# Kernel optimization log

Hardware: AMD Instinct MI355X
Metric: run time of the kernel (lower is better)

## Reference

```python
import jax, jax.numpy as jnp
import numpy as np


def _others_idx(n):
    # idx[i] = all agent indices except i, in order (prev agents then next agents),
    # matching the torch cat([prev_agents_msgs, next_agents_msgs]) ordering.
    return np.array([[j for j in range(n) if j != i] for i in range(n)], dtype=np.int32)


def setup_inputs() -> dict:
    key = jax.random.key(0)
    ks = jax.random.split(key, 6)
    bs, T, n, msg_len, obs_dim, hidden = 64, 256, 8, 16, 128, 64
    in_dim = obs_dim + (n - 1) * msg_len  # 240
    return {
        "obs": jax.random.normal(ks[0], (bs, T, n, obs_dim), jnp.float32),
        "messages": jax.random.normal(ks[1], (bs, T, n, msg_len), jnp.float32),
        "W1": jax.random.normal(ks[2], (n, in_dim, hidden), jnp.float32) * 0.05,
        "b1": jax.random.normal(ks[3], (n, hidden), jnp.float32) * 0.05,
        "W2": jax.random.normal(ks[4], (n, hidden, 1), jnp.float32) * 0.05,
        "b2": jax.random.normal(ks[5], (n, 1), jnp.float32) * 0.05,
    }


def reference(obs, messages, W1, b1, W2, b2):
    bs, T, n, msg_len = messages.shape
    idx = jnp.asarray(_others_idx(n))  # [n, n-1]
    # For each agent i at time t>0: concat of all OTHER agents' messages at t-1.
    m_prev = messages[:, :-1]                      # [bs, T-1, n, msg_len]
    gathered = m_prev[:, :, idx]                   # [bs, T-1, n, n-1, msg_len]
    msgs = gathered.reshape(bs, T - 1, n, (n - 1) * msg_len)
    pad = jnp.zeros((bs, 1, n, (n - 1) * msg_len), msgs.dtype)  # t=0 has no prior msgs
    msgs = jnp.concatenate([pad, msgs], axis=1)    # [bs, T, n, (n-1)*msg_len]
    inputs = jnp.concatenate([obs, msgs], axis=3)  # [bs, T, n, in_dim]
    # Per-agent independent MLP critic: Linear -> ReLU -> Linear
    h = jax.nn.relu(jnp.einsum('btai,aih->btah', inputs, W1) + b1)
    q = jnp.einsum('btah,aho->btao', h, W2) + b2   # [bs, T, n, 1]
    return q
```

## Files before the change

kernel.cpp:

```cpp
#include <hip/hip_runtime.h>


#define NAGENTS 8
#define MSG_LEN 16
#define OBS_DIM 128
#define HIDDEN  64
#define IN_DIM  240
#define TT      256
#define ROWS    16384
#define KSTEPS  15
#define MTILE   256
#define NFRAG   (KSTEPS * 2 * 64 * 8)

typedef __attribute__((ext_vector_type(8)))  short bf16x8;
typedef __attribute__((ext_vector_type(16))) float f32x16;

__device__ __forceinline__ unsigned short f2bf(float x) {
    unsigned u = __float_as_uint(x);
    u += 0x7fffu + ((u >> 16) & 1u);
    return (unsigned short)(u >> 16);
}
__device__ __forceinline__ float bf2f(unsigned short h) {
    return __uint_as_float(((unsigned)h) << 16);
}

__global__ __launch_bounds__(512, 4) void accritic_mfma_kernel(
    const float* __restrict__ obs,
    const float* __restrict__ msgs,
    const float* __restrict__ W1,
    const float* __restrict__ b1,
    const float* __restrict__ W2,
    const float* __restrict__ b2,
    float* __restrict__ out)
{
    __shared__ unsigned short WH[NFRAG];
    __shared__ unsigned short WL[NFRAG];

    const int a   = blockIdx.y;
    const int tid = threadIdx.x;
    const float* __restrict__ w1a = W1 + (size_t)a * IN_DIM * HIDDEN;

#pragma unroll
    for (int i = 0; i < NFRAG / 512; ++i) {
        int e    = tid + i * 512;
        int j    = e & 7;
        int lane = (e >> 3) & 63;
        int nt   = (e >> 9) & 1;
        int ks   = e >> 10;
        int k    = ks * 16 + (lane >> 5) * 8 + j;
        int col  = nt * 32 + (lane & 31);
        float w  = w1a[k * HIDDEN + col];
        unsigned short h = f2bf(w);
        WH[e] = h;
        WL[e] = f2bf(w - bf2f(h));
    }
    __syncthreads();

    const int wv   = tid >> 6;
    const int lane = tid & 63;
    const int rl   = lane & 31;
    const int kg   = lane >> 5;
    const int r    = blockIdx.x * MTILE + wv * 32 + rl;
    const int t    = r & (TT - 1);
    const bool zmsg = (t == 0);
    const int  rs   = zmsg ? r : r - 1;

    const float* __restrict__ obsp = obs + ((size_t)r * NAGENTS + a) * OBS_DIM + kg * 8;
    const float* __restrict__ msgp = msgs + (size_t)rs * NAGENTS * MSG_LEN + kg * 8;

    f32x16 acc0, acc1;
#pragma unroll
    for (int i = 0; i < 16; ++i) { acc0[i] = 0.f; acc1[i] = 0.f; }

    const bf16x8* __restrict__ WH8 = reinterpret_cast<const bf16x8*>(WH);
    const bf16x8* __restrict__ WL8 = reinterpret_cast<const bf16x8*>(WL);

#pragma unroll
    for (int ks = 0; ks < KSTEPS; ++ks) {
        float4 f0, f1;
        if (ks < 8) {
            const float4* p = reinterpret_cast<const float4*>(obsp + ks * 16);
            f0 = p[0]; f1 = p[1];
        } else {
            int pidx = ks - 8;
            int jsrc = (pidx < a) ? pidx : pidx + 1;
            const float4* p = reinterpret_cast<const float4*>(msgp + jsrc * MSG_LEN);
            f0 = p[0]; f1 = p[1];
            if (zmsg) { f0 = make_float4(0.f, 0.f, 0.f, 0.f); f1 = f0; }
        }

        float xf[8] = { f0.x, f0.y, f0.z, f0.w, f1.x, f1.y, f1.z, f1.w };
        bf16x8 ahi, alo;
#pragma unroll
        for (int q = 0; q < 8; ++q) {
            unsigned short h = f2bf(xf[q]);
            ahi[q] = (short)h;
            alo[q] = (short)f2bf(xf[q] - bf2f(h));
        }

        bf16x8 bh0 = WH8[(ks * 2 + 0) * 64 + lane];
        bf16x8 bh1 = WH8[(ks * 2 + 1) * 64 + lane];
        bf16x8 bl0 = WL8[(ks * 2 + 0) * 64 + lane];
        bf16x8 bl1 = WL8[(ks * 2 + 1) * 64 + lane];

        acc0 = __builtin_amdgcn_mfma_f32_32x32x16_bf16(ahi, bh0, acc0, 0, 0, 0);
        acc1 = __builtin_amdgcn_mfma_f32_32x32x16_bf16(ahi, bh1, acc1, 0, 0, 0);
        acc0 = __builtin_amdgcn_mfma_f32_32x32x16_bf16(alo, bh0, acc0, 0, 0, 0);
        acc1 = __builtin_amdgcn_mfma_f32_32x32x16_bf16(alo, bh1, acc1, 0, 0, 0);
        acc0 = __builtin_amdgcn_mfma_f32_32x32x16_bf16(ahi, bl0, acc0, 0, 0, 0);
        acc1 = __builtin_amdgcn_mfma_f32_32x32x16_bf16(ahi, bl1, acc1, 0, 0, 0);
    }

    const int cl = lane & 31;
    const float b1v0 = b1[a * HIDDEN + cl];
    const float b1v1 = b1[a * HIDDEN + 32 + cl];
    const float w2v0 = W2[a * HIDDEN + cl];
    const float w2v1 = W2[a * HIDDEN + 32 + cl];
    const float b2v  = b2[a];

    float v[16];
#pragma unroll
    for (int i = 0; i < 16; ++i) {
        float h0 = fmaxf(acc0[i] + b1v0, 0.f);
        float h1 = fmaxf(acc1[i] + b1v1, 0.f);
        v[i] = h0 * w2v0 + h1 * w2v1;
    }
#pragma unroll
    for (int off = 16; off >= 1; off >>= 1) {
#pragma unroll
        for (int i = 0; i < 16; ++i) v[i] += __shfl_xor(v[i], off, 64);
    }

    if (cl == 0) {
        const int r0 = blockIdx.x * MTILE + wv * 32;
#pragma unroll
        for (int i = 0; i < 16; ++i) {
            int row = (i & 3) + 8 * (i >> 2) + 4 * kg;
            out[(size_t)(r0 + row) * NAGENTS + a] = v[i] + b2v;
        }
    }
}

extern "C" void kernel_launch(void* const* d_in, const int* in_sizes, int n_in,
                              void* d_out, int out_size, void* d_ws, size_t ws_size,
                              hipStream_t stream) {
    const float* obs  = (const float*)d_in[0];
    const float* msgs = (const float*)d_in[1];
    const float* W1   = (const float*)d_in[2];
    const float* b1   = (const float*)d_in[3];
    const float* W2   = (const float*)d_in[4];
    const float* b2   = (const float*)d_in[5];
    float* out = (float*)d_out;

    dim3 grid(ROWS / MTILE, NAGENTS);
    accritic_mfma_kernel<<<grid, dim3(512), 0, stream>>>(obs, msgs, W1, b1, W2, b2, out);
}
```

Baseline: 125.0 us.

## Restructure critic kernel with register-resident weights and prefetched LDS-staged input tiles

Each block now processes four 64-row tiles in sequence. It keeps the W1 hi/lo bf16 fragments in registers rather than LDS, and stages coalesced input loads through LDS as pre-split hi/lo bf16. The next tile's global loads are issued before the current tile's MFMAs so memory latency overlaps compute. The two N halves are split across waves and combined through a small shared buffer, and the hi part now uses truncation instead of rounding. The cost is much higher register pressure (weights plus prefetch buffers) and extra barriers per tile.

```diff
diff --git a/kernel.cpp b/kernel.cpp
--- a/kernel.cpp
+++ b/kernel.cpp
@@ -9,22 +9,114 @@
 #define TT      256
 #define ROWS    16384
 #define KSTEPS  15
-#define MTILE   256
-#define NFRAG   (KSTEPS * 2 * 64 * 8)
+#define MTILE   64
+#define ASTR    248
+#define TPB     4
+#define GX      (ROWS / (MTILE * TPB))
 
 typedef __attribute__((ext_vector_type(8)))  short bf16x8;
 typedef __attribute__((ext_vector_type(16))) float f32x16;
 
-__device__ __forceinline__ unsigned short f2bf(float x) {
+__device__ __forceinline__ unsigned short f2bf_rne(float x) {
     unsigned u = __float_as_uint(x);
     u += 0x7fffu + ((u >> 16) & 1u);
     return (unsigned short)(u >> 16);
 }
-__device__ __forceinline__ float bf2f(unsigned short h) {
-    return __uint_as_float(((unsigned)h) << 16);
+
+__device__ __forceinline__ void load_tile(float4 (&xv)[15],
+    const float* __restrict__ obs, const float* __restrict__ msgs,
+    int m0, int a, int tid)
+{
+#pragma unroll
+    for (int it = 0; it < 15; ++it) {
+        int f4  = tid + it * 256;
+        int row = f4 / 60;
+        int c   = f4 - row * 60;
+        int r   = m0 + row;
+        float4 v;
+        if (c < 32) {
+            v = *reinterpret_cast<const float4*>(
+                    obs + ((size_t)r * NAGENTS + a) * OBS_DIM + c * 4);
+        } else {
+            int p    = (c - 32) >> 2;
+            int jsrc = (p < a) ? p : p + 1;
+            if ((r & (TT - 1)) == 0) {
+                v = make_float4(0.f, 0.f, 0.f, 0.f);
+            } else {
+                v = *reinterpret_cast<const float4*>(
+                        msgs + ((size_t)(r - 1) * NAGENTS + jsrc) * MSG_LEN
+                             + ((c - 32) & 3) * 4);
+            }
+        }
+        xv[it] = v;
+    }
 }
 
-__global__ __launch_bounds__(512, 4) void accritic_mfma_kernel(
+__device__ __forceinline__ void pack_tile(const float4 (&xv)[15],
+    unsigned short* __restrict__ sAH, unsigned short* __restrict__ sAL, int tid)
+{
+#pragma unroll
+    for (int it = 0; it < 15; ++it) {
+        int f4  = tid + it * 256;
+        int row = f4 / 60;
+        int c   = f4 - row * 60;
+        float fv[4] = { xv[it].x, xv[it].y, xv[it].z, xv[it].w };
+        unsigned u[4], h[4]; unsigned short l[4];
+#pragma unroll
+        for (int i = 0; i < 4; ++i) {
+            u[i] = __float_as_uint(fv[i]);
+            h[i] = u[i] & 0xffff0000u;
+            l[i] = f2bf_rne(fv[i] - __uint_as_float(h[i]));
+        }
+        uint2 ph, pl;
+        ph.x = (u[0] >> 16) | h[1];
+        ph.y = (u[2] >> 16) | h[3];
+        pl.x = (unsigned)l[0] | ((unsigned)l[1] << 16);
+        pl.y = (unsigned)l[2] | ((unsigned)l[3] << 16);
+        *reinterpret_cast<uint2*>(&sAH[row * ASTR + c * 4]) = ph;
+        *reinterpret_cast<uint2*>(&sAL[row * ASTR + c * 4]) = pl;
+    }
+}
+
+#define TILE_BODY(XV, XVN, IT, DO_NEXT)                                         \
+    {                                                                           \
+        pack_tile(XV, sAH, sAL, tid);                                           \
+        __syncthreads();                                                        \
+        if (DO_NEXT) load_tile(XVN, obs, msgs, m_base + ((IT) + 1) * MTILE, a, tid); \
+        f32x16 acc;                                                             \
+        _Pragma("unroll")                                                       \
+        for (int i = 0; i < 16; ++i) acc[i] = 0.f;                              \
+        _Pragma("unroll")                                                       \
+        for (int ks = 0; ks < KSTEPS; ++ks) {                                   \
+            int so = arow * ASTR + ks * 16 + kg * 8;                            \
+            bf16x8 ahi = *reinterpret_cast<const bf16x8*>(&sAH[so]);            \
+            bf16x8 alo = *reinterpret_cast<const bf16x8*>(&sAL[so]);            \
+            acc = __builtin_amdgcn_mfma_f32_32x32x16_bf16(ahi, bh[ks], acc, 0, 0, 0); \
+            acc = __builtin_amdgcn_mfma_f32_32x32x16_bf16(alo, bh[ks], acc, 0, 0, 0); \
+            acc = __builtin_amdgcn_mfma_f32_32x32x16_bf16(ahi, bl[ks], acc, 0, 0, 0); \
+        }                                                                       \
+        float v[16];                                                            \
+        _Pragma("unroll")                                                       \
+        for (int i = 0; i < 16; ++i) v[i] = fmaxf(acc[i] + b1v, 0.f) * w2v;     \
+        _Pragma("unroll")                                                       \
+        for (int off = 16; off >= 1; off >>= 1) {                               \
+            _Pragma("unroll")                                                   \
+            for (int i = 0; i < 16; ++i) v[i] += __shfl_xor(v[i], off, 64);     \
+        }                                                                       \
+        if (cl == 0) {                                                          \
+            _Pragma("unroll")                                                   \
+            for (int i = 0; i < 16; ++i) {                                      \
+                int row = (i & 3) + 8 * (i >> 2) + 4 * kg;                      \
+                qp[half * 64 + slab * 32 + row] = v[i];                         \
+            }                                                                   \
+        }                                                                       \
+        __syncthreads();                                                        \
+        if (tid < MTILE)                                                        \
+            out[(size_t)(m_base + (IT) * MTILE + tid) * NAGENTS + a] =          \
+                qp[tid] + qp[64 + tid] + b2v;                                   \
+    }
+
+__global__ __launch_bounds__(256, 2) void accritic_mfma_v5(
     const float* __restrict__ obs,
     const float* __restrict__ msgs,
     const float* __restrict__ W1,
@@ -33,112 +125,52 @@
     const float* __restrict__ b2,
     float* __restrict__ out)
 {
-    __shared__ unsigned short WH[NFRAG];
-    __shared__ unsigned short WL[NFRAG];
+    __shared__ __align__(16) unsigned short sAH[MTILE * ASTR];
+    __shared__ __align__(16) unsigned short sAL[MTILE * ASTR];
+    __shared__ float qp[128];
 
-    const int a   = blockIdx.y;
-    const int tid = threadIdx.x;
+    const int a      = blockIdx.y;
+    const int g      = blockIdx.x;
+    const int tid    = threadIdx.x;
+    const int wv     = tid >> 6;
+    const int lane   = tid & 63;
+    const int slab   = wv & 1;
+    const int half   = wv >> 1;
+    const int rl     = lane & 31;
+    const int kg     = lane >> 5;
+    const int cl     = lane & 31;
+    const int arow   = slab * 32 + rl;
+    const int m_base = g * (MTILE * TPB);
+
+    float4 xv0[15], xv1[15], xv2[15], xv3[15];
+    load_tile(xv0, obs, msgs, m_base, a, tid);
+
     const float* __restrict__ w1a = W1 + (size_t)a * IN_DIM * HIDDEN;
-
-#pragma unroll
-    for (int i = 0; i < NFRAG / 512; ++i) {
-        int e    = tid + i * 512;
-        int j    = e & 7;
-        int lane = (e >> 3) & 63;
-        int nt   = (e >> 9) & 1;
-        int ks   = e >> 10;
-        int k    = ks * 16 + (lane >> 5) * 8 + j;
-        int col  = nt * 32 + (lane & 31);
-        float w  = w1a[k * HIDDEN + col];
-        unsigned short h = f2bf(w);
-        WH[e] = h;
-        WL[e] = f2bf(w - bf2f(h));
-    }
-    __syncthreads();
-
-    const int wv   = tid >> 6;
-    const int lane = tid & 63;
-    const int rl   = lane & 31;
-    const int kg   = lane >> 5;
-    const int r    = blockIdx.x * MTILE + wv * 32 + rl;
-    const int t    = r & (TT - 1);
-    const bool zmsg = (t == 0);
-    const int  rs   = zmsg ? r : r - 1;
-
-    const float* __restrict__ obsp = obs + ((size_t)r * NAGENTS + a) * OBS_DIM + kg * 8;
-    const float* __restrict__ msgp = msgs + (size_t)rs * NAGENTS * MSG_LEN + kg * 8;
-
-    f32x16 acc0, acc1;
-#pragma unroll
-    for (int i = 0; i < 16; ++i) { acc0[i] = 0.f; acc1[i] = 0.f; }
-
-    const bf16x8* __restrict__ WH8 = reinterpret_cast<const bf16x8*>(WH);
-    const bf16x8* __restrict__ WL8 = reinterpret_cast<const bf16x8*>(WL);
-
+    bf16x8 bh[KSTEPS], bl[KSTEPS];
 #pragma unroll
     for (int ks = 0; ks < KSTEPS; ++ks) {
-        float4 f0, f1;
-        if (ks < 8) {
-            const float4* p = reinterpret_cast<const float4*>(obsp + ks * 16);
-            f0 = p[0]; f1 = p[1];
-        } else {
-            int pidx = ks - 8;
-            int jsrc = (pidx < a) ? pidx : pidx + 1;
-            const float4* p = reinterpret_cast<const float4*>(msgp + jsrc * MSG_LEN);
-            f0 = p[0]; f1 = p[1];
-            if (zmsg) { f0 = make_float4(0.f, 0.f, 0.f, 0.f); f1 = f0; }
+        const int kbase = ks * 16 + kg * 8;
+        const int col   = half * 32 + cl;
+        float w[8];
+#pragma unroll
+        for (int j = 0; j < 8; ++j)
+            w[j] = w1a[(size_t)(kbase + j) * HIDDEN + col];
+#pragma unroll
+        for (int j = 0; j < 8; ++j) {
+            unsigned u = __float_as_uint(w[j]);
+            bh[ks][j] = (short)(u >> 16);
+            bl[ks][j] = (short)f2bf_rne(w[j] - __uint_as_float(u & 0xffff0000u));
         }
-
-        float xf[8] = { f0.x, f0.y, f0.z, f0.w, f1.x, f1.y, f1.z, f1.w };
-        bf16x8 ahi, alo;
-#pragma unroll
-        for (int q = 0; q < 8; ++q) {
-            unsigned short h = f2bf(xf[q]);
-            ahi[q] = (short)h;
-            alo[q] = (short)f2bf(xf[q] - bf2f(h));
-        }
-
-        bf16x8 bh0 = WH8[(ks * 2 + 0) * 64 + lane];
-        bf16x8 bh1 = WH8[(ks * 2 + 1) * 64 + lane];
-        bf16x8 bl0 = WL8[(ks * 2 + 0) * 64 + lane];
-        bf16x8 bl1 = WL8[(ks * 2 + 1) * 64 + lane];
-
-        acc0 = __builtin_amdgcn_mfma_f32_32x32x16_bf16(ahi, bh0, acc0, 0, 0, 0);
-        acc1 = __builtin_amdgcn_mfma_f32_32x32x16_bf16(ahi, bh1, acc1, 0, 0, 0);
-        acc0 = __builtin_amdgcn_mfma_f32_32x32x16_bf16(alo, bh0, acc0, 0, 0, 0);
-        acc1 = __builtin_amdgcn_mfma_f32_32x32x16_bf16(alo, bh1, acc1, 0, 0, 0);
-        acc0 = __builtin_amdgcn_mfma_f32_32x32x16_bf16(ahi, bl0, acc0, 0, 0, 0);
-        acc1 = __builtin_amdgcn_mfma_f32_32x32x16_bf16(ahi, bl1, acc1, 0, 0, 0);
     }
 
-    const int cl = lane & 31;
-    const float b1v0 = b1[a * HIDDEN + cl];
-    const float b1v1 = b1[a * HIDDEN + 32 + cl];
-    const float w2v0 = W2[a * HIDDEN + cl];
-    const float w2v1 = W2[a * HIDDEN + 32 + cl];
-    const float b2v  = b2[a];
+    const float b1v = b1[a * HIDDEN + half * 32 + cl];
+    const float w2v = W2[a * HIDDEN + half * 32 + cl];
+    const float b2v = b2[a];
 
-    float v[16];
-#pragma unroll
-    for (int i = 0; i < 16; ++i) {
-        float h0 = fmaxf(acc0[i] + b1v0, 0.f);
-        float h1 = fmaxf(acc1[i] + b1v1, 0.f);
-        v[i] = h0 * w2v0 + h1 * w2v1;
-    }
-#pragma unroll
-    for (int off = 16; off >= 1; off >>= 1) {
-#pragma unroll
-        for (int i = 0; i < 16; ++i) v[i] += __shfl_xor(v[i], off, 64);
-    }
-
-    if (cl == 0) {
-        const int r0 = blockIdx.x * MTILE + wv * 32;
-#pragma unroll
-        for (int i = 0; i < 16; ++i) {
-            int row = (i & 3) + 8 * (i >> 2) + 4 * kg;
-            out[(size_t)(r0 + row) * NAGENTS + a] = v[i] + b2v;
-        }
-    }
+    TILE_BODY(xv0, xv1, 0, true)
+    TILE_BODY(xv1, xv2, 1, true)
+    TILE_BODY(xv2, xv3, 2, true)
+    TILE_BODY(xv3, xv0, 3, false)
 }
 
 extern "C" void kernel_launch(void* const* d_in, const int* in_sizes, int n_in,
@@ -152,6 +184,6 @@
     const float* b2   = (const float*)d_in[5];
     float* out = (float*)d_out;
 
-    dim3 grid(ROWS / MTILE, NAGENTS);
-    accritic_mfma_kernel<<<grid, dim3(512), 0, stream>>>(obs, msgs, W1, b1, W2, b2, out);
+    accritic_mfma_v5<<<dim3(GX, NAGENTS), dim3(256), 0, stream>>>(
+        obs, msgs, W1, b1, W2, b2, out);
 }
```

New measurement: 244.8 us. 1.96x slower.
